# Kernel tuning notes

Hardware: AMD Instinct MI355X
Metric: run time of the kernel (lower is better)

The kernel has to match this reference:

```python
import jax, jax.numpy as jnp
import numpy as np

B, S, D = 2, 2048, 4096
H, KV, HD = 32, 8, 128
THETA = 500000.0


def setup_inputs() -> dict:
    key = jax.random.key(0)
    ks = jax.random.split(key, 5)
    x = jax.random.normal(ks[0], (B, S, D), jnp.float32) * 0.02
    wq = jax.random.normal(ks[1], (H * HD, D), jnp.float32) * 0.02
    wk = jax.random.normal(ks[2], (KV * HD, D), jnp.float32) * 0.02
    wv = jax.random.normal(ks[3], (KV * HD, D), jnp.float32) * 0.02
    wo = jax.random.normal(ks[4], (D, H * HD), jnp.float32) * 0.02
    # HF-style rotary embeddings: cos/sin of shape [B, S, head_dim]
    inv_freq = 1.0 / (THETA ** (jnp.arange(0, HD, 2, dtype=jnp.float32) / HD))
    pos = jnp.arange(S, dtype=jnp.float32)
    freqs = pos[:, None] * inv_freq[None, :]            # [S, HD/2]
    emb = jnp.concatenate([freqs, freqs], axis=-1)      # [S, HD]
    cos = jnp.broadcast_to(jnp.cos(emb)[None], (B, S, HD)).astype(jnp.float32)
    sin = jnp.broadcast_to(jnp.sin(emb)[None], (B, S, HD)).astype(jnp.float32)
    return {"x": x, "wq": wq, "wk": wk, "wv": wv, "wo": wo, "cos": cos, "sin": sin}


def _rotate_half(u):
    return jnp.concatenate([-u[..., HD // 2:], u[..., :HD // 2]], axis=-1)


def reference(x, wq, wk, wv, wo, cos, sin):
    # QKV projections (Linear with weight [out, in], bias=False)
    q = (x @ wq.T).reshape(B, S, H, HD).transpose(0, 2, 1, 3)    # [B,H,S,HD]
    k = (x @ wk.T).reshape(B, S, KV, HD).transpose(0, 2, 1, 3)   # [B,KV,S,HD]
    v = (x @ wv.T).reshape(B, S, KV, HD).transpose(0, 2, 1, 3)   # [B,KV,S,HD]
    # RoPE (rotate_half convention), cos/sin broadcast over heads
    c = cos[:, None, :, :]
    s = sin[:, None, :, :]
    q = q * c + _rotate_half(q) * s
    k = k * c + _rotate_half(k) * s
    # GQA: repeat kv heads
    rep = H // KV
    k = jnp.repeat(k, rep, axis=1)
    v = jnp.repeat(v, rep, axis=1)
    # causal SDPA (attention_mask=None, q_len>1 -> is_causal=True)
    scores = jnp.einsum('bhqd,bhkd->bhqk', q, k) / jnp.sqrt(jnp.float32(HD))
    causal = jnp.tril(jnp.ones((S, S), dtype=bool))
    scores = jnp.where(causal[None, None], scores, jnp.float32(-1e30))
    probs = jax.nn.softmax(scores, axis=-1)
    attn = jnp.einsum('bhqk,bhkd->bhqd', probs, v)
    attn = attn.transpose(0, 2, 1, 3).reshape(B, S, H * HD)
    return attn @ wo.T
```

## Files before the change

### kernel.cpp

```cpp
#include <hip/hip_runtime.h>
#include <hip/hip_bf16.h>

#define B_ 2
#define S_ 2048
#define D_ 4096
#define H_ 32
#define KV_ 8
#define HD_ 128

typedef __attribute__((ext_vector_type(8))) short sh8;
typedef __attribute__((ext_vector_type(4))) short sh4;
typedef __attribute__((ext_vector_type(4))) float f32x4;

__device__ __forceinline__ float b2f(unsigned short u) {
    union { unsigned int i; float f; } v; v.i = ((unsigned)u) << 16; return v.f;
}
__device__ __forceinline__ unsigned short f2b(float f) {
    union { float f; unsigned int i; } v; v.f = f;
    unsigned r = v.i + 0x7fffu + ((v.i >> 16) & 1u);
    return (unsigned short)(r >> 16);
}
__device__ __forceinline__ void gload_lds16(const void* g, void* l) {
    __builtin_amdgcn_global_load_lds((const __attribute__((address_space(1))) void*)g,
                                     (__attribute__((address_space(3))) void*)l, 16, 0, 0);
}

#define BARX() do { asm volatile("" ::: "memory"); __builtin_amdgcn_s_barrier(); asm volatile("" ::: "memory"); } while (0)

__global__ __launch_bounds__(256) void f2b_kernel(const float* __restrict__ in,
                                                  unsigned short* __restrict__ out, int n8) {
    int t = blockIdx.x * 256 + threadIdx.x;
    if (t >= n8) return;
    const float* p = in + (size_t)t * 8;
    float4 a = *(const float4*)p;
    float4 b = *(const float4*)(p + 4);
    sh8 o;
    o[0] = (short)f2b(a.x); o[1] = (short)f2b(a.y); o[2] = (short)f2b(a.z); o[3] = (short)f2b(a.w);
    o[4] = (short)f2b(b.x); o[5] = (short)f2b(b.y); o[6] = (short)f2b(b.z); o[7] = (short)f2b(b.w);
    *(sh8*)(out + (size_t)t * 8) = o;
}

__device__ __forceinline__ void cstore(float* C, size_t i, float v) { C[i] = v; }
__device__ __forceinline__ void cstore(unsigned short* C, size_t i, float v) { C[i] = f2b(v); }

#define MFMAQ(MH, NH)                                                                              \
    do {                                                                                           \
        __builtin_amdgcn_s_setprio(1);                                                             \
        _Pragma("unroll") for (int ks = 0; ks < 2; ks++)                                           \
        _Pragma("unroll") for (int mi = 0; mi < 4; mi++)                                           \
        _Pragma("unroll") for (int ni = 0; ni < 2; ni++)                                           \
            acc[(MH)*4 + mi][(NH)*2 + ni] = __builtin_amdgcn_mfma_f32_16x16x32_bf16(               \
                af[mi][ks], bfr[ni][ks], acc[(MH)*4 + mi][(NH)*2 + ni], 0, 0, 0);                  \
        __builtin_amdgcn_s_setprio(0);                                                             \
    } while (0)

__device__ __forceinline__ void stage2(const unsigned short* s, size_t off128, int tp,
                                       unsigned short* d) {
    const unsigned short* sp = s + (size_t)tp * 64;
    gload_lds16(sp, d);
    gload_lds16(sp + off128, d + 4096);
}

template <typename CT>
__global__ __launch_bounds__(512, 2) void gemm256_bt_kernel(const unsigned short* __restrict__ A,
                                                            const unsigned short* __restrict__ Bm,
                                                            CT* __restrict__ C, int M, int N, int K) {
    __shared__ __align__(16) unsigned short Al[2][2][8192];
    __shared__ __align__(16) unsigned short Bl[2][2][8192];
    const int NT = K >> 6;
    const int nwg = gridDim.x;
    const int wg = blockIdx.x;
    const int cpx = nwg >> 3;
    const int swz = (wg & 7) * cpx + (wg >> 3);
    const int nbn = N >> 8;
    const int bm = swz / nbn, bn = swz % nbn;
    const int T = threadIdx.x;
    const int w = T >> 6, l = T & 63;
    const int wm = w >> 2, wn = w & 3;
    const int fr = l & 15, fq = l >> 4;
    const int u = T >> 3;
    const int swc = ((T & 7) ^ (u & 7)) << 3;
    const size_t Ks = (size_t)K;
    const size_t off128 = 128 * Ks;
    const unsigned short* a0s = A + ((size_t)bm * 256 + u) * Ks + swc;
    const unsigned short* a1s = A + ((size_t)bm * 256 + 64 + u) * Ks + swc;
    const unsigned short* b0s = Bm + ((size_t)bn * 256 + (u >> 5) * 64 + (u & 31)) * Ks + swc;
    const unsigned short* b1s = b0s + 32 * Ks;
    const int T8 = T * 8;
    int aoff[4][2], boff[2][2];
#pragma unroll
    for (int mi = 0; mi < 4; mi++)
#pragma unroll
        for (int ks = 0; ks < 2; ks++)
            aoff[mi][ks] = (wm * 64 + mi * 16 + fr) * 64 + ((((ks << 2) | fq) ^ (fr & 7)) << 3);
#pragma unroll
    for (int ni = 0; ni < 2; ni++)
#pragma unroll
        for (int ks = 0; ks < 2; ks++)
            boff[ni][ks] = (wn * 32 + ni * 16 + fr) * 64 + ((((ks << 2) | fq) ^ (fr & 7)) << 3);
    f32x4 acc[8][4];
#pragma unroll
    for (int i = 0; i < 8; i++)
#pragma unroll
        for (int j = 0; j < 4; j++) acc[i][j] = (f32x4){0.f, 0.f, 0.f, 0.f};

    stage2(a0s, off128, 0, &Al[0][0][T8]);
    stage2(a1s, off128, 0, &Al[0][1][T8]);
    stage2(b0s, off128, 0, &Bl[0][0][T8]);
    stage2(b1s, off128, 0, &Bl[0][1][T8]);
    const int t1c = (NT > 1) ? 1 : 0;
    stage2(a0s, off128, t1c, &Al[1][0][T8]);
    stage2(b1s, off128, t1c, &Bl[1][1][T8]);
    asm volatile("s_waitcnt vmcnt(4)" ::: "memory");
    BARX();

    sh8 af[4][2], bfr[2][2];
    for (int t = 0; t < NT; ++t) {
        const int p = t & 1, pn = p ^ 1;
        const int tp1 = (t + 1 < NT) ? t + 1 : NT - 1;
        const int tp2 = (t + 2 < NT) ? t + 2 : NT - 1;
        const unsigned short* Am0 = &Al[p][0][0];
        const unsigned short* Am1 = &Al[p][1][0];
        const unsigned short* Bn0 = &Bl[p][0][0];
        const unsigned short* Bn1 = &Bl[p][1][0];
#pragma unroll
        for (int mi = 0; mi < 4; mi++) {
            af[mi][0] = *(const sh8*)(Am0 + aoff[mi][0]);
            af[mi][1] = *(const sh8*)(Am0 + aoff[mi][1]);
        }
#pragma unroll
        for (int ni = 0; ni < 2; ni++) {
            bfr[ni][0] = *(const sh8*)(Bn0 + boff[ni][0]);
            bfr[ni][1] = *(const sh8*)(Bn0 + boff[ni][1]);
        }
        stage2(a1s, off128, tp1, &Al[pn][1][T8]);
        BARX();
        MFMAQ(0, 0);
        BARX();
#pragma unroll
        for (int ni = 0; ni < 2; ni++) {
            bfr[ni][0] = *(const sh8*)(Bn1 + boff[ni][0]);
            bfr[ni][1] = *(const sh8*)(Bn1 + boff[ni][1]);
        }
        stage2(b0s, off128, tp1, &Bl[pn][0][T8]);
        BARX();
        MFMAQ(0, 1);
        BARX();
#pragma unroll
        for (int mi = 0; mi < 4; mi++) {
            af[mi][0] = *(const sh8*)(Am1 + aoff[mi][0]);
            af[mi][1] = *(const sh8*)(Am1 + aoff[mi][1]);
        }
        stage2(a0s, off128, tp2, &Al[p][0][T8]);
        BARX();
        MFMAQ(1, 1);
        BARX();
#pragma unroll
        for (int ni = 0; ni < 2; ni++) {
            bfr[ni][0] = *(const sh8*)(Bn0 + boff[ni][0]);
            bfr[ni][1] = *(const sh8*)(Bn0 + boff[ni][1]);
        }
        stage2(b1s, off128, tp2, &Bl[p][1][T8]);
        asm volatile("s_waitcnt vmcnt(4)" ::: "memory");
        BARX();
        MFMAQ(1, 0);
        BARX();
    }
    const size_t crow0 = (size_t)bm * 256 + wm * 128;
    const size_t ccol0 = (size_t)bn * 256 + wn * 64;
#pragma unroll
    for (int mi8 = 0; mi8 < 8; mi8++)
#pragma unroll
        for (int ni4 = 0; ni4 < 4; ni4++) {
            size_t r = crow0 + mi8 * 16 + fq * 4;
            size_t c = ccol0 + ni4 * 16 + fr;
#pragma unroll
            for (int j = 0; j < 4; j++) cstore(C, (r + j) * (size_t)N + c, acc[mi8][ni4][j]);
        }
}

template <int NH>
__global__ __launch_bounds__(256) void rope_kernel(const unsigned short* __restrict__ raw,
                                                   const float* __restrict__ cosb,
                                                   const float* __restrict__ sinb,
                                                   unsigned short* __restrict__ out, float scale,
                                                   int srcOff, int srcStride) {
    int t = blockIdx.x * 256 + threadIdx.x;
    int g = t & 7;
    int h = (t >> 3) & (NH - 1);
    int row = t / (8 * NH);
    if (row >= B_ * S_) return;
    int b = row >> 11, s = row & (S_ - 1);
    const unsigned short* qr = raw + (size_t)row * srcStride + srcOff + h * HD_ + g * 8;
    sh8 lo = *(const sh8*)qr;
    sh8 hi = *(const sh8*)(qr + 64);
    const float* cp = cosb + (size_t)row * HD_ + g * 8;
    const float* sp = sinb + (size_t)row * HD_ + g * 8;
    float4 c0 = *(const float4*)cp, c1 = *(const float4*)(cp + 4);
    float4 s0 = *(const float4*)sp, s1 = *(const float4*)(sp + 4);
    float cc[8] = {c0.x, c0.y, c0.z, c0.w, c1.x, c1.y, c1.z, c1.w};
    float ss[8] = {s0.x, s0.y, s0.z, s0.w, s1.x, s1.y, s1.z, s1.w};
    sh8 olo, ohi;
#pragma unroll
    for (int i = 0; i < 8; i++) {
        float fl = b2f((unsigned short)lo[i]);
        float fh = b2f((unsigned short)hi[i]);
        olo[i] = (short)f2b((fl * cc[i] - fh * ss[i]) * scale);
        ohi[i] = (short)f2b((fh * cc[i] + fl * ss[i]) * scale);
    }
    unsigned short* op = out + (((size_t)b * NH + h) * S_ + s) * HD_ + g * 8;
    *(sh8*)op = olo;
    *(sh8*)(op + 64) = ohi;
}

__global__ __launch_bounds__(256) void vtrans_kernel(const unsigned short* __restrict__ vraw,
                                                     unsigned short* __restrict__ vt) {
    __shared__ unsigned short tile[64][132];
    int bid = blockIdx.x;
    int st = bid & 31;
    int kv = (bid >> 5) & 7;
    int b = bid >> 8;
    int s0 = st * 64;
    int t = threadIdx.x;
    {
        int s = t >> 2, dq = (t & 3) * 32;
        const unsigned short* src = vraw + ((size_t)(b * S_ + s0 + s)) * 6144 + 5120 + kv * HD_ + dq;
#pragma unroll
        for (int i = 0; i < 4; i++) *(sh8*)&tile[s][dq + i * 8] = *(const sh8*)(src + i * 8);
    }
    __syncthreads();
    {
        int d = t & 127, sh = t >> 7;
        unsigned short* dst = vt + (((size_t)(b * KV_ + kv)) * HD_ + d) * S_ + s0 + sh * 32;
#pragma unroll
        for (int q = 0; q < 4; q++) {
            sh8 vv;
#pragma unroll
            for (int e = 0; e < 8; e++) vv[e] = (short)tile[sh * 32 + q * 8 + e][d];
            *(sh8*)(dst + q * 8) = vv;
        }
    }
}

#if __has_builtin(__builtin_amdgcn_mfma_f32_16x16x16bf16_1k)
__device__ __forceinline__ f32x4 pv_mfma(sh4 a, sh4 b, f32x4 c) {
    return __builtin_amdgcn_mfma_f32_16x16x16bf16_1k(a, b, c, 0, 0, 0);
}
#else
__device__ __forceinline__ f32x4 pv_mfma(sh4 a, sh4 b, f32x4 c) {
    sh8 a8 = {a[0], a[1], a[2], a[3], 0, 0, 0, 0};
    sh8 b8 = {b[0], b[1], b[2], b[3], 0, 0, 0, 0};
    return __builtin_amdgcn_mfma_f32_16x16x32_bf16(a8, b8, c, 0, 0, 0);
}
#endif

__global__ __launch_bounds__(256, 4) void attn_kernel(const unsigned short* __restrict__ Q,
                                                      const unsigned short* __restrict__ Kr,
                                                      const unsigned short* __restrict__ Vt,
                                                      unsigned short* __restrict__ O) {
    __shared__ __align__(16) unsigned short Kl[64 * 128];
    __shared__ __align__(16) unsigned short Vl[128 * 64];
    int nwg = gridDim.x;
    int bid0 = blockIdx.x;
    int cpx = nwg >> 3;
    int u = (bid0 & 7) * cpx + (bid0 >> 3);
    int qi = u & 31;
    int h = (u >> 5) & 31;
    int b = u >> 10;
    int kv = h >> 2;
    int t = threadIdx.x, w = t >> 6, l = t & 63;
    int fr = l & 15, fq = l >> 4;
    int qw = qi * 64 + w * 16;
    const unsigned short* Qp = Q + (((size_t)b * H_ + h) * S_ + qw + fr) * HD_;
    sh8 qf[4];
#pragma unroll
    for (int kk = 0; kk < 4; kk++) qf[kk] = *(const sh8*)(Qp + kk * 32 + fq * 8);
    const unsigned short* Kg = Kr + ((size_t)b * KV_ + kv) * S_ * HD_;
    const unsigned short* Vg = Vt + ((size_t)b * KV_ + kv) * HD_ * S_;
    f32x4 po[8];
#pragma unroll
    for (int i = 0; i < 8; i++) po[i] = (f32x4){0.f, 0.f, 0.f, 0.f};
    float m_r = -3.0e38f;
    float l_r = 0.f;
    for (int j = 0; j <= qi; ++j) {
#pragma unroll
        for (int r = 0; r < 4; ++r) {
            int chunk = r * 4 + w;
            {
                int lb = chunk * 1024 + l * 16;
                int srow = lb >> 8;
                int cs = (lb >> 4) & 15;
                int gs = cs ^ (srow & 7);
                const char* ga = (const char*)(Kg + (size_t)(j * 64 + srow) * HD_) + gs * 16;
                gload_lds16(ga, (char*)Kl + chunk * 1024);
            }
            {
                int lb = chunk * 1024 + l * 16;
                int drow = lb >> 7;
                int cs = (lb >> 4) & 7;
                int gs = cs ^ (drow & 7);
                const char* gv = (const char*)(Vg + (size_t)drow * S_ + j * 64 + gs * 8);
                gload_lds16(gv, (char*)Vl + chunk * 1024);
            }
        }
        __syncthreads();
        f32x4 sacc[4];
#pragma unroll
        for (int nc = 0; nc < 4; nc++) {
            sacc[nc] = (f32x4){0.f, 0.f, 0.f, 0.f};
            int n = nc * 16 + fr;
#pragma unroll
            for (int kk = 0; kk < 4; kk++) {
                sh8 kf = *(const sh8*)(Kl + n * 128 + (((kk * 4 + fq) ^ (n & 7)) * 8));
                sacc[nc] = __builtin_amdgcn_mfma_f32_16x16x32_bf16(kf, qf[kk], sacc[nc], 0, 0, 0);
            }
        }
        if (j == qi) {
            int qg = qw + fr;
#pragma unroll
            for (int nc = 0; nc < 4; nc++)
#pragma unroll
                for (int j3 = 0; j3 < 4; j3++) {
                    int kg = j * 64 + nc * 16 + fq * 4 + j3;
                    if (kg > qg) sacc[nc][j3] = -1e30f;
                }
        }
        float tm = sacc[0][0];
#pragma unroll
        for (int nc = 0; nc < 4; nc++)
#pragma unroll
            for (int j3 = 0; j3 < 4; j3++) tm = fmaxf(tm, sacc[nc][j3]);
        tm = fmaxf(tm, __shfl_xor(tm, 16));
        tm = fmaxf(tm, __shfl_xor(tm, 32));
        bool resc = !__all(tm <= m_r + 8.0f);
        if (resc) {
            float nm = fmaxf(m_r, tm);
            float alpha = __expf(m_r - nm);
            m_r = nm;
            l_r *= alpha;
            float aj[4];
#pragma unroll
            for (int j3 = 0; j3 < 4; j3++) aj[j3] = __shfl(alpha, (l & 48) | (fq * 4 + j3));
#pragma unroll
            for (int dc = 0; dc < 8; dc++)
#pragma unroll
                for (int j3 = 0; j3 < 4; j3++) po[dc][j3] *= aj[j3];
        }
        float rs = 0.f;
#pragma unroll
        for (int nc = 0; nc < 4; nc++)
#pragma unroll
            for (int j3 = 0; j3 < 4; j3++) {
                float pv = __expf(sacc[nc][j3] - m_r);
                sacc[nc][j3] = pv;
                rs += pv;
            }
        rs += __shfl_xor(rs, 16);
        rs += __shfl_xor(rs, 32);
        l_r += rs;
        sh4 pa[4];
#pragma unroll
        for (int nc = 0; nc < 4; nc++) {
            unsigned int lo, hi;
            asm("v_cvt_pk_bf16_f32 %0, %1, %2" : "=v"(lo) : "v"(sacc[nc][0]), "v"(sacc[nc][1]));
            asm("v_cvt_pk_bf16_f32 %0, %1, %2" : "=v"(hi) : "v"(sacc[nc][2]), "v"(sacc[nc][3]));
            union { unsigned int u2[2]; sh4 v; } pk;
            pk.u2[0] = lo; pk.u2[1] = hi;
            pa[nc] = pk.v;
        }
#pragma unroll
        for (int dc = 0; dc < 8; dc++) {
            int d = dc * 16 + fr;
#pragma unroll
            for (int nc = 0; nc < 4; nc++) {
                const unsigned short* vp =
                    Vl + d * 64 + (((2 * nc + (fq >> 1)) ^ (d & 7)) * 8) + (fq & 1) * 4;
                sh4 vf = *(const sh4*)vp;
                po[dc] = pv_mfma(pa[nc], vf, po[dc]);
            }
        }
        __syncthreads();
    }
    float il = 1.f / l_r;
    float inj[4];
#pragma unroll
    for (int j3 = 0; j3 < 4; j3++) inj[j3] = __shfl(il, (l & 48) | (fq * 4 + j3));
#pragma unroll
    for (int j3 = 0; j3 < 4; j3++) {
        size_t orow = (size_t)b * S_ + qw + fq * 4 + j3;
#pragma unroll
        for (int dc = 0; dc < 8; dc++)
            O[orow * (H_ * HD_) + h * HD_ + dc * 16 + fr] = f2b(po[dc][j3] * inj[j3]);
    }
}

extern "C" void kernel_launch(void* const* d_in, const int* in_sizes, int n_in,
                              void* d_out, int out_size, void* d_ws, size_t ws_size,
                              hipStream_t stream) {
    const float* x = (const float*)d_in[0];
    const float* wq = (const float*)d_in[1];
    const float* wk = (const float*)d_in[2];
    const float* wv = (const float*)d_in[3];
    const float* wo = (const float*)d_in[4];
    const float* cosb = (const float*)d_in[5];
    const float* sinb = (const float*)d_in[6];
    float* out = (float*)d_out;

    unsigned short* p = (unsigned short*)d_ws;
    unsigned short* xb = p;      p += (size_t)16777216;
    unsigned short* wqkvb = p;   p += (size_t)25165824;
    unsigned short* wob = p;     p += (size_t)16777216;
    unsigned short* qkvraw = p;  p += (size_t)25165824;
    unsigned short* qrope = p;   p += (size_t)16777216;
    unsigned short* krope = p;   p += (size_t)4194304;
    unsigned short* vt = p;      p += (size_t)4194304;
    unsigned short* attnb = p;   p += (size_t)16777216;

    f2b_kernel<<<8192, 256, 0, stream>>>(x, xb, 2097152);
    f2b_kernel<<<8192, 256, 0, stream>>>(wq, wqkvb, 2097152);
    f2b_kernel<<<2048, 256, 0, stream>>>(wk, wqkvb + (size_t)16777216, 524288);
    f2b_kernel<<<2048, 256, 0, stream>>>(wv, wqkvb + (size_t)20971520, 524288);
    f2b_kernel<<<8192, 256, 0, stream>>>(wo, wob, 2097152);

    gemm256_bt_kernel<unsigned short><<<384, 512, 0, stream>>>(xb, wqkvb, qkvraw, 4096, 6144, 4096);

    rope_kernel<32><<<4096, 256, 0, stream>>>(qkvraw, cosb, sinb, qrope, 0.08838834764831845f, 0, 6144);
    rope_kernel<8><<<1024, 256, 0, stream>>>(qkvraw, cosb, sinb, krope, 1.0f, 4096, 6144);
    vtrans_kernel<<<512, 256, 0, stream>>>(qkvraw, vt);

    attn_kernel<<<2048, 256, 0, stream>>>(qrope, krope, vt, attnb);

    gemm256_bt_kernel<float><<<256, 512, 0, stream>>>(attnb, wob, out, 4096, 4096, 4096);
}
```

Before: 827.4 us.

## Stage GEMM epilogue through LDS for vectorized stores and remap tiles to XCDs

The GEMM epilogue now writes each 16-row slice of accumulators into LDS (padded stride 260), then reads back contiguous 16-element chunks and emits 16/32-byte vector global stores instead of scattered scalar stores. Separately, the workgroup-to-tile mapping is changed so each XCD gets an 8-row by N/4-column block of tiles, aiming to improve L2 reuse of A and B per XCD. The epilogue adds extra barriers and LDS traffic. The new mapping hardcodes assumptions about grid and tile counts (bm in 0..15, N divisible by 1024), which may not hold for every GEMM shape.

```diff
diff --git a/kernel.cpp b/kernel.cpp
--- a/kernel.cpp
+++ b/kernel.cpp
@@ -40,9 +40,6 @@
     *(sh8*)(out + (size_t)t * 8) = o;
 }
 
-__device__ __forceinline__ void cstore(float* C, size_t i, float v) { C[i] = v; }
-__device__ __forceinline__ void cstore(unsigned short* C, size_t i, float v) { C[i] = f2b(v); }
-
 #define MFMAQ(MH, NH)                                                                              \
     do {                                                                                           \
         __builtin_amdgcn_s_setprio(1);                                                             \
@@ -68,12 +65,12 @@
     __shared__ __align__(16) unsigned short Al[2][2][8192];
     __shared__ __align__(16) unsigned short Bl[2][2][8192];
     const int NT = K >> 6;
-    const int nwg = gridDim.x;
     const int wg = blockIdx.x;
-    const int cpx = nwg >> 3;
-    const int swz = (wg & 7) * cpx + (wg >> 3);
-    const int nbn = N >> 8;
-    const int bm = swz / nbn, bn = swz % nbn;
+    const int xcd = wg & 7;
+    const int idx = wg >> 3;
+    const int rn = (N >> 8) >> 2;
+    const int bm = ((xcd >> 2) << 3) + (idx & 7);
+    const int bn = (xcd & 3) * rn + (idx >> 3);
     const int T = threadIdx.x;
     const int w = T >> 6, l = T & 63;
     const int wm = w >> 2, wn = w & 3;
@@ -166,17 +163,41 @@
         MFMAQ(1, 0);
         BARX();
     }
-    const size_t crow0 = (size_t)bm * 256 + wm * 128;
-    const size_t ccol0 = (size_t)bn * 256 + wn * 64;
-#pragma unroll
-    for (int mi8 = 0; mi8 < 8; mi8++)
-#pragma unroll
-        for (int ni4 = 0; ni4 < 4; ni4++) {
-            size_t r = crow0 + mi8 * 16 + fq * 4;
-            size_t c = ccol0 + ni4 * 16 + fr;
-#pragma unroll
-            for (int j = 0; j < 4; j++) cstore(C, (r + j) * (size_t)N + c, acc[mi8][ni4][j]);
-        }
+    float* lf = (float*)&Al[0][0][0];
+    const int erow = T & 31;
+    const int ecg = (T >> 5) * 16;
+    const size_t gr0 = (size_t)bm * 256 + (erow >> 4) * 128 + (erow & 15);
+    const size_t gc0 = (size_t)bn * 256 + ecg;
+#pragma unroll
+    for (int mi8 = 0; mi8 < 8; mi8++) {
+        BARX();
+#pragma unroll
+        for (int ni4 = 0; ni4 < 4; ni4++)
+#pragma unroll
+            for (int j = 0; j < 4; j++)
+                lf[(wm * 16 + fq * 4 + j) * 260 + wn * 64 + ni4 * 16 + fr] = acc[mi8][ni4][j];
+        BARX();
+        const float* src = lf + erow * 260 + ecg;
+        float4 f0 = *(const float4*)(src + 0);
+        float4 f1 = *(const float4*)(src + 4);
+        float4 f2 = *(const float4*)(src + 8);
+        float4 f3 = *(const float4*)(src + 12);
+        CT* cp = C + (gr0 + mi8 * 16) * (size_t)N + gc0;
+        if constexpr (sizeof(CT) == 2) {
+            sh8 o0, o1;
+            o0[0] = (short)f2b(f0.x); o0[1] = (short)f2b(f0.y); o0[2] = (short)f2b(f0.z); o0[3] = (short)f2b(f0.w);
+            o0[4] = (short)f2b(f1.x); o0[5] = (short)f2b(f1.y); o0[6] = (short)f2b(f1.z); o0[7] = (short)f2b(f1.w);
+            o1[0] = (short)f2b(f2.x); o1[1] = (short)f2b(f2.y); o1[2] = (short)f2b(f2.z); o1[3] = (short)f2b(f2.w);
+            o1[4] = (short)f2b(f3.x); o1[5] = (short)f2b(f3.y); o1[6] = (short)f2b(f3.z); o1[7] = (short)f2b(f3.w);
+            *(sh8*)(cp) = o0;
+            *(sh8*)(cp + 8) = o1;
+        } else {
+            *(float4*)(cp) = f0;
+            *(float4*)(cp + 4) = f1;
+            *(float4*)(cp + 8) = f2;
+            *(float4*)(cp + 12) = f3;
+        }
+    }
 }
 
 template <int NH>
```

Measured after the change: 852.4 us. 3.0% more time.
